# Kernel optimization log

Hardware: AMD Instinct MI355X
Metric: run time of the kernel (lower is better)

The kernel has to match this reference:

```python
import jax, jax.numpy as jnp
import numpy as np

# dims (match init_kwargs)
N = 262144      # num_memory_locations
D = 128         # dim_memory
C = 512         # dim_controller_output
E_IN = 256      # dim_external_input
OUT = 256       # dim_NTM_output
R = 2           # num_read_heads
WH = 1          # num_write_heads
RAD = 1         # shift_radius
S = 2 * RAD + 1 # shift vector length
EPS = 1e-8


def setup_inputs() -> dict:
    key = jax.random.key(0)
    ks = jax.random.split(key, 40)
    f = lambda i, shape, s=0.05: jax.random.normal(ks[i], shape, dtype=jnp.float32) * s
    inp = {
        "external_input": f(0, (E_IN,), 1.0),
        "M": f(1, (N, D), 1.0),                      # memory matrix
        "prev_read": jnp.zeros((R, D), jnp.float32),  # first step: past readings are zeros
        "Wc": f(2, (C, E_IN + R * D)), "bc": f(3, (C,)),
        "Wo": f(4, (OUT, C + R * D)), "bo": f(5, (OUT,)),
        # read heads (stacked over head axis)
        "rWk": f(6, (R, D, C)),  "rbk": f(7, (R, D)),
        "rWb": f(8, (R, C)),     "rbb": f(9, (R,)),
        "rWg": f(10, (R, C)),    "rbg": f(11, (R,)),
        "rWs": f(12, (R, S, C)), "rbs": f(13, (R, S)),
        "rWgm": f(14, (R, C)),   "rbgm": f(15, (R,)),
        "rinit": f(16, (R, N), 1.0),
        # write heads
        "wWk": f(17, (WH, D, C)),  "wbk": f(18, (WH, D)),
        "wWb": f(19, (WH, C)),     "wbb": f(20, (WH,)),
        "wWg": f(21, (WH, C)),     "wbg": f(22, (WH,)),
        "wWs": f(23, (WH, S, C)),  "wbs": f(24, (WH, S)),
        "wWgm": f(25, (WH, C)),    "wbgm": f(26, (WH,)),
        "wWe": f(27, (WH, D, C)),  "wbe": f(28, (WH, D)),
        "wWa": f(29, (WH, D, C)),  "wba": f(30, (WH, D)),
        "winit": f(31, (WH, N), 1.0),
    }
    return inp


def _address(c, M, Mnorm, w_prev, Wk, bk, Wb, bb, Wg, bg, Ws, bs, Wgm, bgm):
    """Standard NTM addressing: content -> interpolate -> circular shift -> sharpen."""
    k = jnp.tanh(Wk @ c + bk)                       # [D] key
    beta = jax.nn.softplus(Wb @ c + bb)             # scalar key strength
    g = jax.nn.sigmoid(Wg @ c + bg)                 # scalar interpolation gate
    s = jax.nn.softmax(Ws @ c + bs)                 # [S] shift distribution
    gamma = 1.0 + jax.nn.softplus(Wgm @ c + bgm)    # scalar sharpening >= 1
    # content addressing: cosine similarity against all N memory rows
    sim = (M @ k) / (Mnorm * jnp.linalg.norm(k) + EPS)   # [N]
    w_c = jax.nn.softmax(beta * sim)
    # interpolation with previous weighting
    w_g = g * w_c + (1.0 - g) * w_prev
    # circular convolution shift (small fixed radius -> unrolled)
    w_t = jnp.zeros_like(w_g)
    for j, sh in enumerate(range(-RAD, RAD + 1)):
        w_t = w_t + s[j] * jnp.roll(w_g, sh)
    # sharpening
    w_p = w_t ** gamma
    return w_p / (w_p.sum() + EPS)


_address_heads = jax.vmap(_address, in_axes=(None, None, None, 0, 0, 0, 0, 0, 0, 0, 0, 0, 0, 0))


def reference(external_input, M, prev_read, Wc, bc, Wo, bo,
              rWk, rbk, rWb, rbb, rWg, rbg, rWs, rbs, rWgm, rbgm, rinit,
              wWk, wbk, wWb, wbb, wWg, wbg, wWs, wbs, wWgm, wbgm,
              wWe, wbe, wWa, wba, winit):
    # controller
    c = Wc @ jnp.concatenate([external_input, prev_read.reshape(-1)]) + bc   # [C]
    Mnorm = jnp.linalg.norm(M, axis=1)                                        # [N]
    # read heads: addressing (initial weighting = softmax of learned logits) then read
    w_prev_r = jax.nn.softmax(rinit, axis=1)
    read_w = _address_heads(c, M, Mnorm, w_prev_r,
                            rWk, rbk, rWb, rbb, rWg, rbg, rWs, rbs, rWgm, rbgm)  # [R, N]
    readings = read_w @ M                                                     # [R, D]
    # write heads: all weightings computed on pre-write memory
    w_prev_w = jax.nn.softmax(winit, axis=1)
    write_w = _address_heads(c, M, Mnorm, w_prev_w,
                             wWk, wbk, wWb, wbb, wWg, wbg, wWs, wbs, wWgm, wbgm)  # [WH, N]
    # sequential erase-then-add writes
    M_new = M
    for i in range(WH):
        e = jax.nn.sigmoid(wWe[i] @ c + wbe[i])   # [D] erase vector
        a = jnp.tanh(wWa[i] @ c + wba[i])          # [D] add vector
        w = write_w[i][:, None]                    # [N, 1]
        M_new = M_new * (1.0 - w * e[None, :]) + w * a[None, :]
    # NTM output
    out = Wo @ jnp.concatenate([c, readings.reshape(-1)]) + bo               # [OUT]
    return out, readings, read_w, write_w, M_new
```

## Files before the change

### kernel.cpp

```cpp
#include <hip/hip_runtime.h>
#include <hip/hip_bf16.h>

#define NN 262144
#define EPS 1e-8f

#define WS_C      0
#define WS_K      512
#define WS_E      896
#define WS_A      1024
#define WS_KNSQ   1152
#define WS_BETA   1155
#define WS_G      1158
#define WS_GAMMA  1161
#define WS_SL     1164
#define WS_ZC     1173
#define WS_SUMP   1179
#define WS_RDACC  1182
#define WS_T      2048
#define WS_NEEDED ((size_t)(WS_T + 3 * NN) * 4)

#define OUT_OUT   0
#define OUT_READ  256
#define OUT_RW    512
#define OUT_WW    (512 + 2 * NN)
#define OUT_MNEW  ((size_t)(512 + 3 * NN))

__global__ void FFNTM_78477642433000_kernel(int* p) { if (p) *p = 0; }

__device__ __forceinline__ float4 ld4(const float* p) { return *reinterpret_cast<const float4*>(p); }

__device__ __forceinline__ float wred(float v) {
#pragma unroll
    for (int off = 32; off > 0; off >>= 1) v += __shfl_xor(v, off);
    return v;
}

__device__ __forceinline__ void load_shift_params(const float* __restrict__ ws,
        float g[3], float gam[3], float izc[3], float izp[3],
        float s0[3], float s1[3], float s2[3]) {
#pragma unroll
    for (int h = 0; h < 3; h++) {
        g[h]   = ws[WS_G + h];
        gam[h] = ws[WS_GAMMA + h];
        izc[h] = 1.0f / fmaxf(ws[WS_ZC + h],     1e-30f);
        izp[h] = 1.0f / fmaxf(ws[WS_ZC + 3 + h], 1e-30f);
        const float l0 = ws[WS_SL + h*3], l1 = ws[WS_SL + h*3 + 1], l2 = ws[WS_SL + h*3 + 2];
        const float mx = fmaxf(l0, fmaxf(l1, l2));
        const float e0 = expf(l0 - mx), e1 = expf(l1 - mx), e2 = expf(l2 - mx);
        const float inv = 1.0f / (e0 + e1 + e2);
        s0[h] = e0 * inv; s1[h] = e1 * inv; s2[h] = e2 * inv;
    }
}

__global__ void csent(float* out, float val) {
    if (threadIdx.x == 0 && blockIdx.x == 0) out[OUT_OUT] = val;
}

__global__ void __launch_bounds__(256) c0(const float* __restrict__ ei, const float* __restrict__ pr,
                                          const float* __restrict__ Wc, const float* __restrict__ bc,
                                          float* __restrict__ ws) {
    const int t = threadIdx.x;
    const int lane = t & 63;
    const int j = (blockIdx.x * 256 + t) >> 6;

    if (blockIdx.x == 0) {
        for (int i = t; i < 286; i += 256) ws[WS_KNSQ + i] = 0.0f;
    }

    const float* xs = (lane < 32) ? (ei + lane * 8) : (pr + (lane - 32) * 8);
    const float4 xa = ld4(xs), xb = ld4(xs + 4);
    const float* wr = Wc + j * 512 + lane * 8;
    const float4 wa = ld4(wr), wb = ld4(wr + 4);
    float acc = xa.x * wa.x + xa.y * wa.y + xa.z * wa.z + xa.w * wa.w
              + xb.x * wb.x + xb.y * wb.y + xb.z * wb.z + xb.w * wb.w;
    acc = wred(acc);
    if (lane == 0) ws[WS_C + j] = acc + bc[j];
}

__global__ void __launch_bounds__(256) c1(
    const float* __restrict__ rWk, const float* __restrict__ rbk,
    const float* __restrict__ rWb, const float* __restrict__ rbb,
    const float* __restrict__ rWg, const float* __restrict__ rbg,
    const float* __restrict__ rWs, const float* __restrict__ rbs,
    const float* __restrict__ rWgm, const float* __restrict__ rbgm,
    const float* __restrict__ wWk, const float* __restrict__ wbk,
    const float* __restrict__ wWb, const float* __restrict__ wbb,
    const float* __restrict__ wWg, const float* __restrict__ wbg,
    const float* __restrict__ wWs, const float* __restrict__ wbs,
    const float* __restrict__ wWgm, const float* __restrict__ wbgm,
    const float* __restrict__ wWe, const float* __restrict__ wbe,
    const float* __restrict__ wWa, const float* __restrict__ wba,
    float* __restrict__ ws) {
    const int w = blockIdx.x * 4 + (threadIdx.x >> 6);
    const int lane = threadIdx.x & 63;
    if (w >= 658) return;

    const float4 ca = ld4(ws + WS_C + lane * 8);
    const float4 cb = ld4(ws + WS_C + lane * 8 + 4);

    const float* row; float bias; int kind; int h = 0, d = 0, sidx = 0;
    if (w < 384) {
        h = w >> 7; d = w & 127;
        row  = (h < 2) ? (rWk + (h * 128 + d) * 512) : (wWk + d * 512);
        bias = (h < 2) ? rbk[h * 128 + d] : wbk[d];
        kind = 0;
    } else if (w < 512) {
        d = w - 384; row = wWe + d * 512; bias = wbe[d]; kind = 1;
    } else if (w < 640) {
        d = w - 512; row = wWa + d * 512; bias = wba[d]; kind = 2;
    } else if (w < 643) {
        h = w - 640; row = (h < 2) ? (rWb + h * 512) : wWb;
        bias = (h < 2) ? rbb[h] : wbb[0]; kind = 3;
    } else if (w < 646) {
        h = w - 643; row = (h < 2) ? (rWg + h * 512) : wWg;
        bias = (h < 2) ? rbg[h] : wbg[0]; kind = 4;
    } else if (w < 649) {
        h = w - 646; row = (h < 2) ? (rWgm + h * 512) : wWgm;
        bias = (h < 2) ? rbgm[h] : wbgm[0]; kind = 5;
    } else {
        sidx = w - 649; h = sidx / 3; const int jj = sidx % 3;
        row  = (h < 2) ? (rWs + (h * 3 + jj) * 512) : (wWs + jj * 512);
        bias = (h < 2) ? rbs[h * 3 + jj] : wbs[jj];
        kind = 6;
    }

    const float4 ra = ld4(row + lane * 8);
    const float4 rb = ld4(row + lane * 8 + 4);
    float acc = ca.x * ra.x + ca.y * ra.y + ca.z * ra.z + ca.w * ra.w
              + cb.x * rb.x + cb.y * rb.y + cb.z * rb.z + cb.w * rb.w;
    acc = wred(acc);

    if (lane == 0) {
        const float x = acc + bias;
        switch (kind) {
            case 0: { float kv = tanhf(x); ws[WS_K + w] = kv; atomicAdd(&ws[WS_KNSQ + h], kv * kv); } break;
            case 1: ws[WS_E + d] = 1.0f / (1.0f + expf(-x)); break;
            case 2: ws[WS_A + d] = tanhf(x); break;
            case 3: ws[WS_BETA + h] = log1pf(expf(x)); break;
            case 4: ws[WS_G + h] = 1.0f / (1.0f + expf(-x)); break;
            case 5: ws[WS_GAMMA + h] = 1.0f + log1pf(expf(x)); break;
            case 6: ws[WS_SL + sidx] = x; break;
        }
    }
}

__global__ void __launch_bounds__(256) c2(const float* __restrict__ M, const float* __restrict__ rinit,
                                          const float* __restrict__ winit, float* __restrict__ ws) {
    const int t = threadIdx.x;
    const int lane = t & 63;
    const int wv = t >> 6;
    const int grp = t >> 5;
    const int sub = lane & 31;

    float kf0[4], kf1[4], kf2[4];
#pragma unroll
    for (int j = 0; j < 4; j++) {
        kf0[j] = ws[WS_K +       sub * 4 + j];
        kf1[j] = ws[WS_K + 128 + sub * 4 + j];
        kf2[j] = ws[WS_K + 256 + sub * 4 + j];
    }
    float beta[3], kn[3];
#pragma unroll
    for (int h = 0; h < 3; h++) { kn[h] = sqrtf(ws[WS_KNSQ + h]); beta[h] = ws[WS_BETA + h]; }

    float zc0 = 0, zc1 = 0, zc2 = 0, zp0 = 0, zp1 = 0, zp2 = 0;

    for (int row = blockIdx.x * 8 + grp; row < NN; row += gridDim.x * 8) {
        const float4 m = ld4(M + (size_t)row * 128 + sub * 4);
        float d0 = m.x * kf0[0] + m.y * kf0[1] + m.z * kf0[2] + m.w * kf0[3];
        float d1 = m.x * kf1[0] + m.y * kf1[1] + m.z * kf1[2] + m.w * kf1[3];
        float d2 = m.x * kf2[0] + m.y * kf2[1] + m.z * kf2[2] + m.w * kf2[3];
        float ns = m.x * m.x + m.y * m.y + m.z * m.z + m.w * m.w;
#pragma unroll
        for (int off = 1; off < 32; off <<= 1) {
            d0 += __shfl_xor(d0, off);
            d1 += __shfl_xor(d1, off);
            d2 += __shfl_xor(d2, off);
            ns += __shfl_xor(ns, off);
        }
        if (sub == 0) {
            const float mn = sqrtf(ns);
            const float t0 = expf(beta[0] * d0 / (mn * kn[0] + EPS));
            const float t1 = expf(beta[1] * d1 / (mn * kn[1] + EPS));
            const float t2 = expf(beta[2] * d2 / (mn * kn[2] + EPS));
            ws[WS_T + row]          = t0;
            ws[WS_T + NN + row]     = t1;
            ws[WS_T + 2 * NN + row] = t2;
            zc0 += t0; zc1 += t1; zc2 += t2;
        }
    }

    for (int i = blockIdx.x * 256 + t; i < NN; i += gridDim.x * 256) {
        zp0 += expf(rinit[i]);
        zp1 += expf(rinit[NN + i]);
        zp2 += expf(winit[i]);
    }

    __shared__ float red[4][6];
    float vals[6] = {zc0, zc1, zc2, zp0, zp1, zp2};
#pragma unroll
    for (int q = 0; q < 6; q++) {
        float v = wred(vals[q]);
        if (lane == 0) red[wv][q] = v;
    }
    __syncthreads();
    if (t < 6) {
        atomicAdd(&ws[WS_ZC + t], red[0][t] + red[1][t] + red[2][t] + red[3][t]);
    }
}

__global__ void __launch_bounds__(256) c3(const float* __restrict__ rinit, const float* __restrict__ winit,
                                          float* __restrict__ ws) {
    float g[3], gam[3], izc[3], izp[3], s0[3], s1[3], s2[3];
    load_shift_params(ws, g, gam, izc, izp, s0, s1, s2);

    float sump[3] = {0.f, 0.f, 0.f};
    for (int i = blockIdx.x * 256 + threadIdx.x; i < NN; i += gridDim.x * 256) {
        const int im = (i == 0) ? (NN - 1) : (i - 1);
        const int ip = (i == NN - 1) ? 0 : (i + 1);
#pragma unroll
        for (int h = 0; h < 3; h++) {
            const float* init = (h == 0) ? rinit : (h == 1) ? (rinit + NN) : winit;
            const float* tp = ws + WS_T + h * NN;
            const float gg = g[h], om = 1.0f - gg;
            const float wgm = gg * tp[im] * izc[h] + om * expf(init[im]) * izp[h];
            const float wg0 = gg * tp[i]  * izc[h] + om * expf(init[i])  * izp[h];
            const float wgp = gg * tp[ip] * izc[h] + om * expf(init[ip]) * izp[h];
            const float wt = fmaxf(s0[h] * wgp + s1[h] * wg0 + s2[h] * wgm, 1e-30f);
            sump[h] += expf(gam[h] * logf(wt));
        }
    }

    __shared__ float red[4][3];
    const int lane = threadIdx.x & 63, wv = threadIdx.x >> 6;
#pragma unroll
    for (int h = 0; h < 3; h++) {
        float v = wred(sump[h]);
        if (lane == 0) red[wv][h] = v;
    }
    __syncthreads();
    if (threadIdx.x < 3) {
        atomicAdd(&ws[WS_SUMP + threadIdx.x],
                  red[0][threadIdx.x] + red[1][threadIdx.x] + red[2][threadIdx.x] + red[3][threadIdx.x]);
    }
}

__global__ void __launch_bounds__(256) c4(const float* __restrict__ M, const float* __restrict__ rinit,
                                          const float* __restrict__ winit, float* __restrict__ out,
                                          float* __restrict__ ws) {
    float g[3], gam[3], izc[3], izp[3], s0[3], s1[3], s2[3];
    load_shift_params(ws, g, gam, izc, izp, s0, s1, s2);
    float isp[3];
#pragma unroll
    for (int h = 0; h < 3; h++) isp[h] = 1.0f / (ws[WS_SUMP + h] + EPS);

    const int t = threadIdx.x;
    const int lane = t & 63;
    const int wv = t >> 6;
    const int grp = t >> 5;
    const int sub = lane & 31;

    float ev[4], av[4];
#pragma unroll
    for (int j = 0; j < 4; j++) { ev[j] = ws[WS_E + sub * 4 + j]; av[j] = ws[WS_A + sub * 4 + j]; }

    float r0[4] = {0, 0, 0, 0}, r1[4] = {0, 0, 0, 0};

    for (int row = blockIdx.x * 8 + grp; row < NN; row += gridDim.x * 8) {
        const int im = (row == 0) ? (NN - 1) : (row - 1);
        const int ip = (row == NN - 1) ? 0 : (row + 1);
        float w[3];
#pragma unroll
        for (int h = 0; h < 3; h++) {
            const float* init = (h == 0) ? rinit : (h == 1) ? (rinit + NN) : winit;
            const float* tp = ws + WS_T + h * NN;
            const float gg = g[h], om = 1.0f - gg;
            const float wgm = gg * tp[im]  * izc[h] + om * expf(init[im])  * izp[h];
            const float wg0 = gg * tp[row] * izc[h] + om * expf(init[row]) * izp[h];
            const float wgp = gg * tp[ip]  * izc[h] + om * expf(init[ip])  * izp[h];
            const float wt = fmaxf(s0[h] * wgp + s1[h] * wg0 + s2[h] * wgm, 1e-30f);
            w[h] = expf(gam[h] * logf(wt)) * isp[h];
        }
        const float4 m = ld4(M + (size_t)row * 128 + sub * 4);
        float4 nv;
        nv.x = m.x * (1.0f - w[2] * ev[0]) + w[2] * av[0];
        nv.y = m.y * (1.0f - w[2] * ev[1]) + w[2] * av[1];
        nv.z = m.z * (1.0f - w[2] * ev[2]) + w[2] * av[2];
        nv.w = m.w * (1.0f - w[2] * ev[3]) + w[2] * av[3];
        *reinterpret_cast<float4*>(out + OUT_MNEW + (size_t)row * 128 + sub * 4) = nv;
        r0[0] += w[0] * m.x; r0[1] += w[0] * m.y; r0[2] += w[0] * m.z; r0[3] += w[0] * m.w;
        r1[0] += w[1] * m.x; r1[1] += w[1] * m.y; r1[2] += w[1] * m.z; r1[3] += w[1] * m.w;
        if (sub == 0) {
            out[OUT_RW + row]      = w[0];
            out[OUT_RW + NN + row] = w[1];
            out[OUT_WW + row]      = w[2];
        }
    }

#pragma unroll
    for (int j = 0; j < 4; j++) {
        r0[j] += __shfl_xor(r0[j], 32);
        r1[j] += __shfl_xor(r1[j], 32);
    }
    __shared__ float lds[4][256];
    if (lane < 32) {
#pragma unroll
        for (int j = 0; j < 4; j++) {
            lds[wv][sub * 4 + j]       = r0[j];
            lds[wv][128 + sub * 4 + j] = r1[j];
        }
    }
    __syncthreads();
    atomicAdd(&ws[WS_RDACC + t], lds[0][t] + lds[1][t] + lds[2][t] + lds[3][t]);
}

__global__ void __launch_bounds__(256) c5(const float* __restrict__ Wo, const float* __restrict__ bo,
                                          float* __restrict__ ws, float* __restrict__ out) {
    const int t = threadIdx.x;
    const int lane = t & 63;
    const int j = blockIdx.x * 4 + (t >> 6);
    const float* row = Wo + j * 768;
    float acc = 0.0f;
#pragma unroll
    for (int q = 0; q < 12; q++) {
        const int i = lane * 12 + q;
        const float x = (i < 512) ? ws[WS_C + i] : ws[WS_RDACC + i - 512];
        acc += row[i] * x;
    }
    acc = wred(acc);
    if (lane == 0) out[OUT_OUT + j] = acc + bo[j];
    if (blockIdx.x == 0) out[OUT_READ + t] = ws[WS_RDACC + t];
}

extern "C" void kernel_launch(void* const* d_in, const int* in_sizes, int n_in,
                              void* d_out, int out_size, void* d_ws, size_t ws_size,
                              hipStream_t stream) {
    float* out = (float*)d_out;

    static const int expect[33] = {
        256, 33554432, 256, 262144, 512, 196608, 256,
        131072, 256, 1024, 2, 1024, 2, 3072, 6, 1024, 2, 524288,
        65536, 128, 512, 1, 512, 1, 1536, 3, 512, 1,
        65536, 128, 65536, 128, 262144
    };
    int bad = (n_in == 33) ? -1 : 33;
    if (bad < 0) {
        for (int i = 0; i < 33; i++) {
            if (in_sizes[i] != expect[i]) { bad = i; break; }
        }
    }
    if (bad >= 0) { csent<<<1, 64, 0, stream>>>(out, 10000.0f + (float)bad); return; }
    if (ws_size < WS_NEEDED) { csent<<<1, 64, 0, stream>>>(out, 5000.0f + (float)(ws_size >> 20)); return; }

    const float* ei    = (const float*)d_in[0];
    const float* M     = (const float*)d_in[1];
    const float* pr    = (const float*)d_in[2];
    const float* Wc    = (const float*)d_in[3];
    const float* bc    = (const float*)d_in[4];
    const float* Wo    = (const float*)d_in[5];
    const float* bo    = (const float*)d_in[6];
    const float* rWk   = (const float*)d_in[7];
    const float* rbk   = (const float*)d_in[8];
    const float* rWb   = (const float*)d_in[9];
    const float* rbb   = (const float*)d_in[10];
    const float* rWg   = (const float*)d_in[11];
    const float* rbg   = (const float*)d_in[12];
    const float* rWs   = (const float*)d_in[13];
    const float* rbs   = (const float*)d_in[14];
    const float* rWgm  = (const float*)d_in[15];
    const float* rbgm  = (const float*)d_in[16];
    const float* rinit = (const float*)d_in[17];
    const float* wWk   = (const float*)d_in[18];
    const float* wbk   = (const float*)d_in[19];
    const float* wWb   = (const float*)d_in[20];
    const float* wbb   = (const float*)d_in[21];
    const float* wWg   = (const float*)d_in[22];
    const float* wbg   = (const float*)d_in[23];
    const float* wWs   = (const float*)d_in[24];
    const float* wbs   = (const float*)d_in[25];
    const float* wWgm  = (const float*)d_in[26];
    const float* wbgm  = (const float*)d_in[27];
    const float* wWe   = (const float*)d_in[28];
    const float* wbe   = (const float*)d_in[29];
    const float* wWa   = (const float*)d_in[30];
    const float* wba   = (const float*)d_in[31];
    const float* winit = (const float*)d_in[32];
    float* ws = (float*)d_ws;

    c0<<<128, 256, 0, stream>>>(ei, pr, Wc, bc, ws);
    c1<<<165, 256, 0, stream>>>(rWk, rbk, rWb, rbb, rWg, rbg, rWs, rbs, rWgm, rbgm,
                                wWk, wbk, wWb, wbb, wWg, wbg, wWs, wbs, wWgm, wbgm,
                                wWe, wbe, wWa, wba, ws);
    c2<<<2048, 256, 0, stream>>>(M, rinit, winit, ws);
    c3<<<1024, 256, 0, stream>>>(rinit, winit, ws);
    c4<<<1024, 256, 0, stream>>>(M, rinit, winit, out, ws);
    c5<<<64, 256, 0, stream>>>(Wo, bo, ws, out);
}
```

Baseline: 421.0 us.

## Cache exp(init) and unnormalized weights; spread atomics across replicated slots

c2 now stores exp(rinit/winit) into scratch space in the M_new output region, and c3 reads it there instead of recomputing expf. c3 also writes the unnormalized sharpened weights to the output, so c4 only rescales them rather than redoing the shift and sharpen per row. Atomic reductions are spread over 16 or 8 replicated slots and summed by small extra kernels, which cuts contention. The cost is extra global traffic, two more launches, and reliance on c4 overwriting the scratch region it reuses.

New measurement: 354.7 us. -15.7%, faster.

```diff
diff --git a/kernel.cpp b/kernel.cpp
--- a/kernel.cpp
+++ b/kernel.cpp
@@ -13,10 +13,13 @@
 #define WS_G      1158
 #define WS_GAMMA  1161
 #define WS_SL     1164
-#define WS_ZC     1173
-#define WS_SUMP   1179
-#define WS_RDACC  1182
-#define WS_T      2048
+#define WS_ZC     1184
+#define WS_SUMP   1190
+#define WS_ZCR    1280
+#define WS_SUMPR  1792
+#define WS_RDACC  2304
+#define WS_ZERO_CNT (WS_RDACC + 2048 - WS_KNSQ)
+#define WS_T      4608
 #define WS_NEEDED ((size_t)(WS_T + 3 * NN) * 4)
 
 #define OUT_OUT   0
@@ -64,7 +67,7 @@
     const int j = (blockIdx.x * 256 + t) >> 6;
 
     if (blockIdx.x == 0) {
-        for (int i = t; i < 286; i += 256) ws[WS_KNSQ + i] = 0.0f;
+        for (int i = t; i < WS_ZERO_CNT; i += 256) ws[WS_KNSQ + i] = 0.0f;
     }
 
     const float* xs = (lane < 32) ? (ei + lane * 8) : (pr + (lane - 32) * 8);
@@ -145,7 +148,8 @@
 }
 
 __global__ void __launch_bounds__(256) c2(const float* __restrict__ M, const float* __restrict__ rinit,
-                                          const float* __restrict__ winit, float* __restrict__ ws) {
+                                          const float* __restrict__ winit, float* __restrict__ out,
+                                          float* __restrict__ ws) {
     const int t = threadIdx.x;
     const int lane = t & 63;
     const int wv = t >> 6;
@@ -190,10 +194,15 @@
         }
     }
 
+    float* Esc = out + OUT_MNEW;
     for (int i = blockIdx.x * 256 + t; i < NN; i += gridDim.x * 256) {
-        zp0 += expf(rinit[i]);
-        zp1 += expf(rinit[NN + i]);
-        zp2 += expf(winit[i]);
+        const float e0 = expf(rinit[i]);
+        const float e1 = expf(rinit[NN + i]);
+        const float e2 = expf(winit[i]);
+        Esc[i]          = e0;
+        Esc[NN + i]     = e1;
+        Esc[2 * NN + i] = e2;
+        zp0 += e0; zp1 += e1; zp2 += e2;
     }
 
     __shared__ float red[4][6];
@@ -205,14 +214,25 @@
     }
     __syncthreads();
     if (t < 6) {
-        atomicAdd(&ws[WS_ZC + t], red[0][t] + red[1][t] + red[2][t] + red[3][t]);
-    }
-}
-
-__global__ void __launch_bounds__(256) c3(const float* __restrict__ rinit, const float* __restrict__ winit,
-                                          float* __restrict__ ws) {
+        atomicAdd(&ws[WS_ZCR + (blockIdx.x & 15) * 32 + t],
+                  red[0][t] + red[1][t] + red[2][t] + red[3][t]);
+    }
+}
+
+__global__ void c2b(float* __restrict__ ws) {
+    const int t = threadIdx.x;
+    if (t < 6) {
+        float s = 0.0f;
+#pragma unroll
+        for (int r = 0; r < 16; r++) s += ws[WS_ZCR + r * 32 + t];
+        ws[WS_ZC + t] = s;
+    }
+}
+
+__global__ void __launch_bounds__(256) c3(float* __restrict__ out, float* __restrict__ ws) {
     float g[3], gam[3], izc[3], izp[3], s0[3], s1[3], s2[3];
     load_shift_params(ws, g, gam, izc, izp, s0, s1, s2);
+    const float* Esc = out + OUT_MNEW;
 
     float sump[3] = {0.f, 0.f, 0.f};
     for (int i = blockIdx.x * 256 + threadIdx.x; i < NN; i += gridDim.x * 256) {
@@ -220,14 +240,17 @@
         const int ip = (i == NN - 1) ? 0 : (i + 1);
 #pragma unroll
         for (int h = 0; h < 3; h++) {
-            const float* init = (h == 0) ? rinit : (h == 1) ? (rinit + NN) : winit;
             const float* tp = ws + WS_T + h * NN;
+            const float* Ep = Esc + (size_t)h * NN;
             const float gg = g[h], om = 1.0f - gg;
-            const float wgm = gg * tp[im] * izc[h] + om * expf(init[im]) * izp[h];
-            const float wg0 = gg * tp[i]  * izc[h] + om * expf(init[i])  * izp[h];
-            const float wgp = gg * tp[ip] * izc[h] + om * expf(init[ip]) * izp[h];
+            const float wgm = gg * tp[im] * izc[h] + om * Ep[im] * izp[h];
+            const float wg0 = gg * tp[i]  * izc[h] + om * Ep[i]  * izp[h];
+            const float wgp = gg * tp[ip] * izc[h] + om * Ep[ip] * izp[h];
             const float wt = fmaxf(s0[h] * wgp + s1[h] * wg0 + s2[h] * wgm, 1e-30f);
-            sump[h] += expf(gam[h] * logf(wt));
+            const float p = expf(gam[h] * logf(wt));
+            sump[h] += p;
+            float* pd = (h == 0) ? (out + OUT_RW) : (h == 1) ? (out + OUT_RW + NN) : (out + OUT_WW);
+            pd[i] = p;
         }
     }
 
@@ -240,16 +263,23 @@
     }
     __syncthreads();
     if (threadIdx.x < 3) {
-        atomicAdd(&ws[WS_SUMP + threadIdx.x],
+        atomicAdd(&ws[WS_SUMPR + (blockIdx.x & 15) * 32 + threadIdx.x],
                   red[0][threadIdx.x] + red[1][threadIdx.x] + red[2][threadIdx.x] + red[3][threadIdx.x]);
     }
 }
 
-__global__ void __launch_bounds__(256) c4(const float* __restrict__ M, const float* __restrict__ rinit,
-                                          const float* __restrict__ winit, float* __restrict__ out,
+__global__ void c3b(float* __restrict__ ws) {
+    const int t = threadIdx.x;
+    if (t < 3) {
+        float s = 0.0f;
+#pragma unroll
+        for (int r = 0; r < 16; r++) s += ws[WS_SUMPR + r * 32 + t];
+        ws[WS_SUMP + t] = s;
+    }
+}
+
+__global__ void __launch_bounds__(256) c4(const float* __restrict__ M, float* __restrict__ out,
                                           float* __restrict__ ws) {
-    float g[3], gam[3], izc[3], izp[3], s0[3], s1[3], s2[3];
-    load_shift_params(ws, g, gam, izc, izp, s0, s1, s2);
     float isp[3];
 #pragma unroll
     for (int h = 0; h < 3; h++) isp[h] = 1.0f / (ws[WS_SUMP + h] + EPS);
@@ -267,33 +297,22 @@
     float r0[4] = {0, 0, 0, 0}, r1[4] = {0, 0, 0, 0};
 
     for (int row = blockIdx.x * 8 + grp; row < NN; row += gridDim.x * 8) {
-        const int im = (row == 0) ? (NN - 1) : (row - 1);
-        const int ip = (row == NN - 1) ? 0 : (row + 1);
-        float w[3];
-#pragma unroll
-        for (int h = 0; h < 3; h++) {
-            const float* init = (h == 0) ? rinit : (h == 1) ? (rinit + NN) : winit;
-            const float* tp = ws + WS_T + h * NN;
-            const float gg = g[h], om = 1.0f - gg;
-            const float wgm = gg * tp[im]  * izc[h] + om * expf(init[im])  * izp[h];
-            const float wg0 = gg * tp[row] * izc[h] + om * expf(init[row]) * izp[h];
-            const float wgp = gg * tp[ip]  * izc[h] + om * expf(init[ip])  * izp[h];
-            const float wt = fmaxf(s0[h] * wgp + s1[h] * wg0 + s2[h] * wgm, 1e-30f);
-            w[h] = expf(gam[h] * logf(wt)) * isp[h];
-        }
+        const float w0 = out[OUT_RW + row]      * isp[0];
+        const float w1 = out[OUT_RW + NN + row] * isp[1];
+        const float w2 = out[OUT_WW + row]      * isp[2];
         const float4 m = ld4(M + (size_t)row * 128 + sub * 4);
         float4 nv;
-        nv.x = m.x * (1.0f - w[2] * ev[0]) + w[2] * av[0];
-        nv.y = m.y * (1.0f - w[2] * ev[1]) + w[2] * av[1];
-        nv.z = m.z * (1.0f - w[2] * ev[2]) + w[2] * av[2];
-        nv.w = m.w * (1.0f - w[2] * ev[3]) + w[2] * av[3];
+        nv.x = m.x * (1.0f - w2 * ev[0]) + w2 * av[0];
+        nv.y = m.y * (1.0f - w2 * ev[1]) + w2 * av[1];
+        nv.z = m.z * (1.0f - w2 * ev[2]) + w2 * av[2];
+        nv.w = m.w * (1.0f - w2 * ev[3]) + w2 * av[3];
         *reinterpret_cast<float4*>(out + OUT_MNEW + (size_t)row * 128 + sub * 4) = nv;
-        r0[0] += w[0] * m.x; r0[1] += w[0] * m.y; r0[2] += w[0] * m.z; r0[3] += w[0] * m.w;
-        r1[0] += w[1] * m.x; r1[1] += w[1] * m.y; r1[2] += w[1] * m.z; r1[3] += w[1] * m.w;
+        r0[0] += w0 * m.x; r0[1] += w0 * m.y; r0[2] += w0 * m.z; r0[3] += w0 * m.w;
+        r1[0] += w1 * m.x; r1[1] += w1 * m.y; r1[2] += w1 * m.z; r1[3] += w1 * m.w;
         if (sub == 0) {
-            out[OUT_RW + row]      = w[0];
-            out[OUT_RW + NN + row] = w[1];
-            out[OUT_WW + row]      = w[2];
+            out[OUT_RW + row]      = w0;
+            out[OUT_RW + NN + row] = w1;
+            out[OUT_WW + row]      = w2;
         }
     }
 
@@ -311,12 +330,22 @@
         }
     }
     __syncthreads();
-    atomicAdd(&ws[WS_RDACC + t], lds[0][t] + lds[1][t] + lds[2][t] + lds[3][t]);
+    atomicAdd(&ws[WS_RDACC + (blockIdx.x & 7) * 256 + t],
+              lds[0][t] + lds[1][t] + lds[2][t] + lds[3][t]);
 }
 
 __global__ void __launch_bounds__(256) c5(const float* __restrict__ Wo, const float* __restrict__ bo,
                                           float* __restrict__ ws, float* __restrict__ out) {
-    const int t = threadIdx.x;
+    __shared__ float rd[256];
+    const int t = threadIdx.x;
+    {
+        float s = 0.0f;
+#pragma unroll
+        for (int r = 0; r < 8; r++) s += ws[WS_RDACC + r * 256 + t];
+        rd[t] = s;
+    }
+    __syncthreads();
+
     const int lane = t & 63;
     const int j = blockIdx.x * 4 + (t >> 6);
     const float* row = Wo + j * 768;
@@ -324,12 +353,12 @@
 #pragma unroll
     for (int q = 0; q < 12; q++) {
         const int i = lane * 12 + q;
-        const float x = (i < 512) ? ws[WS_C + i] : ws[WS_RDACC + i - 512];
+        const float x = (i < 512) ? ws[WS_C + i] : rd[i - 512];
         acc += row[i] * x;
     }
     acc = wred(acc);
     if (lane == 0) out[OUT_OUT + j] = acc + bo[j];
-    if (blockIdx.x == 0) out[OUT_READ + t] = ws[WS_RDACC + t];
+    if (blockIdx.x == 0) out[OUT_READ + t] = rd[t];
 }
 
 extern "C" void kernel_launch(void* const* d_in, const int* in_sizes, int n_in,
@@ -391,8 +420,10 @@
     c1<<<165, 256, 0, stream>>>(rWk, rbk, rWb, rbb, rWg, rbg, rWs, rbs, rWgm, rbgm,
                                 wWk, wbk, wWb, wbb, wWg, wbg, wWs, wbs, wWgm, wbgm,
                                 wWe, wbe, wWa, wba, ws);
-    c2<<<2048, 256, 0, stream>>>(M, rinit, winit, ws);
-    c3<<<1024, 256, 0, stream>>>(rinit, winit, ws);
-    c4<<<1024, 256, 0, stream>>>(M, rinit, winit, out, ws);
+    c2<<<2048, 256, 0, stream>>>(M, rinit, winit, out, ws);
+    c2b<<<1, 64, 0, stream>>>(ws);
+    c3<<<1024, 256, 0, stream>>>(out, ws);
+    c3b<<<1, 64, 0, stream>>>(ws);
+    c4<<<1024, 256, 0, stream>>>(M, out, ws);
     c5<<<64, 256, 0, stream>>>(Wo, bo, ws, out);
 }
```
